# Optimization experiments

Measured on AMD Instinct MI355X. Metric: run time of the kernel, lower is better.

The kernel has to match this reference:

```python
import jax, jax.numpy as jnp
import numpy as np

N, Lq, Lk, D = 4, 2048, 2048, 1024
H, DH = 16, 64  # n_heads, projection_dim
NEG_INF = jnp.float32(-1e30)


def setup_inputs() -> dict:
    key = jax.random.key(0)
    ks = jax.random.split(key, 6)
    query = jax.random.normal(ks[0], (N, Lq, D), dtype=jnp.float32)
    key_t = jax.random.normal(ks[1], (N, Lk, D), dtype=jnp.float32)
    s = 1.0 / np.sqrt(D)
    Wq = jax.random.normal(ks[2], (D, D), dtype=jnp.float32) * s
    Wk = jax.random.normal(ks[3], (D, D), dtype=jnp.float32) * s
    Wv = jax.random.normal(ks[4], (D, D), dtype=jnp.float32) * s
    # causal mask: True where attention is forbidden (j > i)
    mask = jnp.triu(jnp.ones((Lq, Lk), dtype=bool), k=1)
    # per-sample valid lengths in [1024, 2048); padding at the tail
    valid_len = jax.random.randint(ks[5], (N,), Lk // 2, Lk)
    padding_mask = jnp.arange(Lk)[None, :] >= valid_len[:, None]  # (N, Lk) bool
    return {"query": query, "key": key_t, "Wq": Wq, "Wk": Wk, "Wv": Wv,
            "mask": mask, "padding_mask": padding_mask}


def reference(query, key, Wq, Wk, Wv, mask, padding_mask):
    n, lq, _ = query.shape
    lk = key.shape[1]
    # torch Linear (no bias): x @ W.T ; split heads -> (N, H, L, DH)
    q = (query @ Wq.T).reshape(n, lq, H, DH).transpose(0, 2, 1, 3)
    k = (key @ Wk.T).reshape(n, lk, H, DH).transpose(0, 2, 1, 3)
    v = (key @ Wv.T).reshape(n, lk, H, DH).transpose(0, 2, 1, 3)
    # per-sample scaling: sqrt(number of non-padded keys) (module quirk, not sqrt(d))
    valid = jnp.sum(~padding_mask, axis=-1).astype(query.dtype)  # (N,)
    scaling = jnp.sqrt(valid)[:, None, None, None]
    score = jnp.einsum('nhqd,nhkd->nhqk', q, k) / scaling
    score = jnp.where(mask[None, None, :, :], NEG_INF, score)
    score = jnp.where(padding_mask[:, None, None, :], NEG_INF, score)
    attn = jax.nn.softmax(score, axis=-1)
    out = jnp.einsum('nhqk,nhkd->nhqd', attn, v)
    return out.transpose(0, 2, 1, 3).reshape(n, lq, H * DH)
```

## Files before the change

### kernel.cpp

```cpp
#include <hip/hip_runtime.h>
#include <hip/hip_bf16.h>
#include <math.h>


#define N_S 4
#define LQ 2048
#define LK 2048
#define DM 1024
#define NHEAD 16
#define DHEAD 64

typedef __attribute__((ext_vector_type(8))) short short8;
typedef __attribute__((ext_vector_type(4))) float f32x4;

typedef const __attribute__((address_space(1))) void* gptr_t;
typedef __attribute__((address_space(3))) void* lptr_t;

#define GLOAD_LDS(g, l) \
    __builtin_amdgcn_global_load_lds((gptr_t)(const void*)(g), (lptr_t)(void*)(l), 16, 0, 0)

static __device__ __forceinline__ unsigned int pkbf(float a, float b) {
    __hip_bfloat162 h = __float22bfloat162_rn(make_float2(a, b));
    unsigned int u;
    __builtin_memcpy(&u, &h, 4);
    return u;
}

static __device__ __forceinline__ f32x4 zero4() {
    f32x4 v; v[0] = 0.f; v[1] = 0.f; v[2] = 0.f; v[3] = 0.f; return v;
}

__global__ void meta_kernel(const void* __restrict__ pm,
                            int* __restrict__ valid_out,
                            float* __restrict__ scale_out) {
    __shared__ int okInt, hasPair, okF32;
    __shared__ int counts[4];
    int t = threadIdx.x;
    if (t == 0) { okInt = 1; hasPair = 0; okF32 = 1; }
    if (t < 4) counts[t] = 0;
    __syncthreads();

    const unsigned int* w = (const unsigned int*)pm;
    int bad_int = 0, pair = 0, bad_f32 = 0;
    for (int i = t; i < 2048; i += 256) {
        unsigned int v = w[i];
        if (v > 1u) bad_int = 1;
        if (v == 0x3F803F80u) pair = 1;
        if (v != 0u && v != 0x3F800000u) bad_f32 = 1;
    }
    if (bad_int) okInt = 0;
    if (pair)    hasPair = 1;
    if (bad_f32) okF32 = 0;
    __syncthreads();

    int mode = okInt ? 0 : (hasPair ? 1 : (okF32 ? 2 : 3));
    for (int n = 0; n < 4; n++) {
        int cnt = 0;
        for (int j = t; j < LK; j += 256) {
            int idx = n * LK + j;
            bool z;
            if (mode == 0)      z = (((const int*)pm)[idx] == 0);
            else if (mode == 1) z = (((const unsigned short*)pm)[idx] == 0);
            else if (mode == 2) z = (w[idx] == 0u);
            else                z = (((const unsigned char*)pm)[idx] == 0);
            cnt += z ? 1 : 0;
        }
        atomicAdd(&counts[n], cnt);
    }
    __syncthreads();
    if (t < 4) {
        int c = counts[t] > 0 ? counts[t] : 1;
        valid_out[t] = c;
        scale_out[t] = 1.0f / sqrtf((float)c);
    }
}

static __device__ __forceinline__ void conv16(const float* src,
                                              unsigned short* dst, size_t idx) {
    f32x4 a0 = *(const f32x4*)(src + idx);
    f32x4 a1 = *(const f32x4*)(src + idx + 4);
    f32x4 a2 = *(const f32x4*)(src + idx + 8);
    f32x4 a3 = *(const f32x4*)(src + idx + 12);
    uint4 u0, u1;
    u0.x = pkbf(a0[0], a0[1]); u0.y = pkbf(a0[2], a0[3]);
    u0.z = pkbf(a1[0], a1[1]); u0.w = pkbf(a1[2], a1[3]);
    u1.x = pkbf(a2[0], a2[1]); u1.y = pkbf(a2[2], a2[3]);
    u1.z = pkbf(a3[0], a3[1]); u1.w = pkbf(a3[2], a3[3]);
    *(uint4*)(void*)(dst + idx) = u0;
    *(uint4*)(void*)(dst + idx + 8) = u1;
}

__global__ __launch_bounds__(256) void convw_kernel(
    const float* __restrict__ Wq, const float* __restrict__ Wk,
    const float* __restrict__ Wv,
    unsigned short* __restrict__ Wqb, unsigned short* __restrict__ Wkb,
    unsigned short* __restrict__ Wvb)
{
    int z = blockIdx.y;
    const float* src = (z == 0) ? Wq : ((z == 1) ? Wk : Wv);
    unsigned short* dst = (z == 0) ? Wqb : ((z == 1) ? Wkb : Wvb);
    conv16(src, dst, ((size_t)blockIdx.x * 256 + threadIdx.x) * 16);
}

__global__ __launch_bounds__(256) void convx_kernel(
    const float* __restrict__ src, unsigned short* __restrict__ dst)
{
    conv16(src, dst, ((size_t)blockIdx.x * 256 + threadIdx.x) * 16);
}

__global__ __launch_bounds__(256) void convx2_kernel(
    const float* __restrict__ q, const float* __restrict__ k,
    unsigned short* __restrict__ dq, unsigned short* __restrict__ dk)
{
    const float* src = blockIdx.y ? k : q;
    unsigned short* dst = blockIdx.y ? dk : dq;
    conv16(src, dst, ((size_t)blockIdx.x * 256 + threadIdx.x) * 16);
}

__global__ __launch_bounds__(256) void proj_bf16_kernel(
    const unsigned short* __restrict__ XbQ, const unsigned short* __restrict__ XbK,
    const unsigned short* __restrict__ Wqb, const unsigned short* __restrict__ Wkb,
    const unsigned short* __restrict__ Wvb,
    const float* __restrict__ scal,
    unsigned short* __restrict__ Qb, unsigned short* __restrict__ Kb,
    unsigned short* __restrict__ Vt, int zbase)
{
    int z = blockIdx.z + zbase;
    const unsigned short* W = (z == 0) ? Wqb : ((z == 1) ? Wkb : Wvb);
    const unsigned short* Xb = (z == 0) ? XbQ : XbK;

    __shared__ unsigned short Xls[128 * 32];
    __shared__ unsigned short Wls[128 * 32];

    int t = threadIdx.x;
    int wave = t >> 6, lane = t & 63;
    int l15 = lane & 15, quad = lane >> 4;
    int wa = wave >> 1, wb = wave & 1;
    int m0 = blockIdx.x << 7, n0 = blockIdx.y << 7;

    int srow = t >> 2;
    int sg = ((t & 3) ^ (srow & 3)) << 3;
    const unsigned short* gX0 = Xb + (size_t)(m0 + srow) * DM + sg;
    const unsigned short* gX1 = Xb + (size_t)(m0 + 64 + srow) * DM + sg;
    const unsigned short* gW0 = W + (size_t)(n0 + srow) * DM + sg;
    const unsigned short* gW1 = W + (size_t)(n0 + 64 + srow) * DM + sg;

    f32x4 acc[4][4];
    #pragma unroll
    for (int i = 0; i < 4; i++)
        #pragma unroll
        for (int j = 0; j < 4; j++) acc[i][j] = zero4();

    int aoff = ((quad ^ (l15 & 3)) << 3);
    const unsigned short* Abuf = (z < 2) ? Wls : Xls;
    const unsigned short* Bbuf = (z < 2) ? Xls : Wls;

    for (int kk = 0; kk < DM; kk += 32) {
        __syncthreads();
        GLOAD_LDS(gX0 + kk, Xls + wave * 512);
        GLOAD_LDS(gX1 + kk, Xls + 2048 + wave * 512);
        GLOAD_LDS(gW0 + kk, Wls + wave * 512);
        GLOAD_LDS(gW1 + kk, Wls + 2048 + wave * 512);
        __syncthreads();

        short8 af[4], bf[4];
        #pragma unroll
        for (int ai = 0; ai < 4; ai++)
            af[ai] = *(const short8*)(const void*)(
                Abuf + ((wa * 64 + ai * 16 + l15) << 5) + aoff);
        #pragma unroll
        for (int bi = 0; bi < 4; bi++)
            bf[bi] = *(const short8*)(const void*)(
                Bbuf + ((wb * 64 + bi * 16 + l15) << 5) + aoff);
        #pragma unroll
        for (int ai = 0; ai < 4; ai++)
            #pragma unroll
            for (int bi = 0; bi < 4; bi++)
                acc[ai][bi] = __builtin_amdgcn_mfma_f32_16x16x32_bf16(
                    af[ai], bf[bi], acc[ai][bi], 0, 0, 0);
    }

    if (z < 2) {
        unsigned short* O = (z == 0) ? Qb : Kb;
        #pragma unroll
        for (int bi = 0; bi < 4; bi++) {
            int token = m0 + wb * 64 + bi * 16 + l15;
            float qs = 1.0f;
            if (z == 0) qs = scal[token >> 11] * 1.44269504f;
            #pragma unroll
            for (int ai = 0; ai < 4; ai++) {
                int feat = n0 + wa * 64 + ai * 16 + quad * 4;
                float v0 = acc[ai][bi][0], v1 = acc[ai][bi][1];
                float v2 = acc[ai][bi][2], v3 = acc[ai][bi][3];
                if (z == 0) { v0 *= qs; v1 *= qs; v2 *= qs; v3 *= qs; }
                uint2 u;
                u.x = pkbf(v0, v1);
                u.y = pkbf(v2, v3);
                *(uint2*)(void*)(O + (size_t)token * DM + feat) = u;
            }
        }
    } else {
        #pragma unroll
        for (int ai = 0; ai < 4; ai++) {
            int token0 = m0 + wa * 64 + ai * 16 + quad * 4;
            int n = token0 >> 11, tl = token0 & 2047;
            #pragma unroll
            for (int bi = 0; bi < 4; bi++) {
                int feat = n0 + wb * 64 + bi * 16 + l15;
                uint2 u;
                u.x = pkbf(acc[ai][bi][0], acc[ai][bi][1]);
                u.y = pkbf(acc[ai][bi][2], acc[ai][bi][3]);
                *(uint2*)(void*)(Vt + ((size_t)n * DM + feat) * LK + tl) = u;
            }
        }
    }
}

__global__ __launch_bounds__(256) void proj_f32_kernel(
    const float* __restrict__ Xq, const float* __restrict__ Xk,
    const unsigned short* __restrict__ Wqb, const unsigned short* __restrict__ Wkb,
    const unsigned short* __restrict__ Wvb,
    const float* __restrict__ scal,
    unsigned short* __restrict__ Qb, unsigned short* __restrict__ Kb,
    unsigned short* __restrict__ Vt)
{
    int z = blockIdx.z;
    const float* X = (z == 0) ? Xq : Xk;
    const unsigned short* W = (z == 0) ? Wqb : ((z == 1) ? Wkb : Wvb);

    __shared__ unsigned short Xls[128 * 32];
    __shared__ unsigned short Wls[128 * 32];

    int t = threadIdx.x;
    int wave = t >> 6, lane = t & 63;
    int l15 = lane & 15, quad = lane >> 4;
    int wa = wave >> 1, wb = wave & 1;
    int m0 = blockIdx.x << 7, n0 = blockIdx.y << 7;

    int arow = t >> 1, ah = t & 1;
    int ag0 = ((2 * ah)     ^ (arow & 3)) << 3;
    int ag1 = ((2 * ah + 1) ^ (arow & 3)) << 3;
    const float* gX = X + (size_t)(m0 + arow) * DM;
    unsigned short* lX = Xls + arow * 32 + ah * 16;

    int brow = t >> 2;
    int bg = ((t & 3) ^ (brow & 3)) << 3;
    const unsigned short* gW0 = W + (size_t)(n0 + brow) * DM + bg;
    const unsigned short* gW1 = W + (size_t)(n0 + 64 + brow) * DM + bg;

    f32x4 acc[4][4];
    #pragma unroll
    for (int i = 0; i < 4; i++)
        #pragma unroll
        for (int j = 0; j < 4; j++) acc[i][j] = zero4();

    int aoff = ((quad ^ (l15 & 3)) << 3);

    f32x4 an0 = *(const f32x4*)(gX + ag0);
    f32x4 an1 = *(const f32x4*)(gX + ag0 + 4);
    f32x4 an2 = *(const f32x4*)(gX + ag1);
    f32x4 an3 = *(const f32x4*)(gX + ag1 + 4);

    const unsigned short* Abuf = (z < 2) ? Wls : Xls;
    const unsigned short* Bbuf = (z < 2) ? Xls : Wls;

    for (int kk = 0; kk < DM; kk += 32) {
        __syncthreads();
        GLOAD_LDS(gW0 + kk, Wls + wave * 512);
        GLOAD_LDS(gW1 + kk, Wls + 2048 + wave * 512);
        uint4 ua, ub;
        ua.x = pkbf(an0[0], an0[1]); ua.y = pkbf(an0[2], an0[3]);
        ua.z = pkbf(an1[0], an1[1]); ua.w = pkbf(an1[2], an1[3]);
        ub.x = pkbf(an2[0], an2[1]); ub.y = pkbf(an2[2], an2[3]);
        ub.z = pkbf(an3[0], an3[1]); ub.w = pkbf(an3[2], an3[3]);
        *(uint4*)(void*)(lX)     = ua;
        *(uint4*)(void*)(lX + 8) = ub;
        __syncthreads();

        if (kk + 32 < DM) {
            an0 = *(const f32x4*)(gX + kk + 32 + ag0);
            an1 = *(const f32x4*)(gX + kk + 32 + ag0 + 4);
            an2 = *(const f32x4*)(gX + kk + 32 + ag1);
            an3 = *(const f32x4*)(gX + kk + 32 + ag1 + 4);
        }

        short8 af[4], bf[4];
        #pragma unroll
        for (int ai = 0; ai < 4; ai++)
            af[ai] = *(const short8*)(const void*)(
                Abuf + ((wa * 64 + ai * 16 + l15) << 5) + aoff);
        #pragma unroll
        for (int bi = 0; bi < 4; bi++)
            bf[bi] = *(const short8*)(const void*)(
                Bbuf + ((wb * 64 + bi * 16 + l15) << 5) + aoff);
        #pragma unroll
        for (int ai = 0; ai < 4; ai++)
            #pragma unroll
            for (int bi = 0; bi < 4; bi++)
                acc[ai][bi] = __builtin_amdgcn_mfma_f32_16x16x32_bf16(
                    af[ai], bf[bi], acc[ai][bi], 0, 0, 0);
    }

    if (z < 2) {
        unsigned short* O = (z == 0) ? Qb : Kb;
        #pragma unroll
        for (int bi = 0; bi < 4; bi++) {
            int token = m0 + wb * 64 + bi * 16 + l15;
            float qs = 1.0f;
            if (z == 0) qs = scal[token >> 11] * 1.44269504f;
            #pragma unroll
            for (int ai = 0; ai < 4; ai++) {
                int feat = n0 + wa * 64 + ai * 16 + quad * 4;
                float v0 = acc[ai][bi][0], v1 = acc[ai][bi][1];
                float v2 = acc[ai][bi][2], v3 = acc[ai][bi][3];
                if (z == 0) { v0 *= qs; v1 *= qs; v2 *= qs; v3 *= qs; }
                uint2 u;
                u.x = pkbf(v0, v1);
                u.y = pkbf(v2, v3);
                *(uint2*)(void*)(O + (size_t)token * DM + feat) = u;
            }
        }
    } else {
        #pragma unroll
        for (int ai = 0; ai < 4; ai++) {
            int token0 = m0 + wa * 64 + ai * 16 + quad * 4;
            int n = token0 >> 11, tl = token0 & 2047;
            #pragma unroll
            for (int bi = 0; bi < 4; bi++) {
                int feat = n0 + wb * 64 + bi * 16 + l15;
                uint2 u;
                u.x = pkbf(acc[ai][bi][0], acc[ai][bi][1]);
                u.y = pkbf(acc[ai][bi][2], acc[ai][bi][3]);
                *(uint2*)(void*)(Vt + ((size_t)n * DM + feat) * LK + tl) = u;
            }
        }
    }
}

__global__ __launch_bounds__(256) void attn_kernel(
    const unsigned short* __restrict__ Qb, const unsigned short* __restrict__ Kb,
    const unsigned short* __restrict__ Vt,
    const int* __restrict__ valid_arr,
    float* __restrict__ out)
{
    __shared__ unsigned short Kls[2][64 * 64];

    int bx = blockIdx.x;
    int nh = blockIdx.y;
    int n = nh >> 4, h = nh & 15;
    int tA = bx, tB = 31 - bx;

    int valid = valid_arr[n];
    int tvalid = (valid + 63) >> 6;
    int TlA = (tA + 1 < tvalid) ? tA + 1 : tvalid;
    int TlB = (tB + 1 < tvalid) ? tB + 1 : tvalid;

    int t = threadIdx.x;
    int wave = t >> 6, lane = t & 63;
    int l15 = lane & 15, quad = lane >> 4;

    int qyA = tA * 64 + wave * 16 + l15;
    int qyB = tB * 64 + wave * 16 + l15;
    int qw0A = tA * 64 + wave * 16;
    int qw0B = tB * 64 + wave * 16;

    const unsigned short* QrowA = Qb + ((size_t)n * LQ + qyA) * DM + h * DHEAD;
    const unsigned short* QrowB = Qb + ((size_t)n * LQ + qyB) * DM + h * DHEAD;
    short8 qfA0 = *(const short8*)(const void*)(QrowA + quad * 8);
    short8 qfA1 = *(const short8*)(const void*)(QrowA + 32 + quad * 8);
    short8 qfB0 = *(const short8*)(const void*)(QrowB + quad * 8);
    short8 qfB1 = *(const short8*)(const void*)(QrowB + 32 + quad * 8);

    f32x4 OA[4], OB[4];
    #pragma unroll
    for (int i = 0; i < 4; i++) { OA[i] = zero4(); OB[i] = zero4(); }
    f32x4 LAcc = zero4(), LBcc = zero4();

    short8 onesf;
    #pragma unroll
    for (int i = 0; i < 8; i++) onesf[i] = (short)0x3F80;

    const unsigned short* Kbase = Kb + (size_t)n * LK * DM + h * DHEAD;
    const unsigned short* Vbase = Vt + ((size_t)n * DM + h * DHEAD) * LK;

    int srow0 = t >> 3;
    int sgk   = (((t & 7) ^ (srow0 & 7)) << 3);

    GLOAD_LDS(Kbase + (size_t)srow0 * DM + sgk,        &Kls[0][0] + wave * 512);
    GLOAD_LDS(Kbase + (size_t)(32 + srow0) * DM + sgk, &Kls[0][0] + 2048 + wave * 512);

    for (int kt = 0; kt < TlB; kt++) {
        int jb = kt << 6;
        int cur = kt & 1;
        bool doA = (kt < TlA);

        __syncthreads();

        f32x4 sA[4], sB[4];
        #pragma unroll
        for (int cb = 0; cb < 4; cb++) {
            const unsigned short* krow = &Kls[cur][0] + ((cb * 16 + l15) << 6);
            short8 kf0 = *(const short8*)(const void*)(krow + ((quad ^ (l15 & 7)) << 3));
            short8 kf1 = *(const short8*)(const void*)(krow + (((4 + quad) ^ (l15 & 7)) << 3));
            f32x4 sb = zero4();
            sb = __builtin_amdgcn_mfma_f32_16x16x32_bf16(kf0, qfB0, sb, 0, 0, 0);
            sb = __builtin_amdgcn_mfma_f32_16x16x32_bf16(kf1, qfB1, sb, 0, 0, 0);
            sB[cb] = sb;
            if (doA) {
                f32x4 sa = zero4();
                sa = __builtin_amdgcn_mfma_f32_16x16x32_bf16(kf0, qfA0, sa, 0, 0, 0);
                sa = __builtin_amdgcn_mfma_f32_16x16x32_bf16(kf1, qfA1, sa, 0, 0, 0);
                sA[cb] = sa;
            }
        }

        short8 vf0[4], vf1[4];
        #pragma unroll
        for (int cb = 0; cb < 4; cb++) {
            vf0[cb] = *(const short8*)(const void*)(
                Vbase + (size_t)(cb * 16 + l15) * LK + jb + quad * 8);
            vf1[cb] = *(const short8*)(const void*)(
                Vbase + (size_t)(cb * 16 + l15) * LK + jb + 32 + quad * 8);
        }
        if (kt + 1 < TlB) {
            int jb2 = jb + 64;
            GLOAD_LDS(Kbase + (size_t)(jb2 + srow0) * DM + sgk,
                      &Kls[1 - cur][0] + wave * 512);
            GLOAD_LDS(Kbase + (size_t)(jb2 + 32 + srow0) * DM + sgk,
                      &Kls[1 - cur][0] + 2048 + wave * 512);
        }

        if (jb + 63 > qw0B || jb + 64 > valid) {
            #pragma unroll
            for (int cb = 0; cb < 4; cb++) {
                int jb2 = jb + cb * 16 + quad * 4;
                #pragma unroll
                for (int r = 0; r < 4; r++) {
                    int j = jb2 + r;
                    if (j > qyB || j >= valid) sB[cb][r] = -1e30f;
                }
            }
        }
        short8 pfB0, pfB1;
        {
            unsigned int lo[4], hi[4];
            #pragma unroll
            for (int cb = 0; cb < 4; cb++) {
                lo[cb] = pkbf(__builtin_amdgcn_exp2f(sB[cb][0]),
                              __builtin_amdgcn_exp2f(sB[cb][1]));
                hi[cb] = pkbf(__builtin_amdgcn_exp2f(sB[cb][2]),
                              __builtin_amdgcn_exp2f(sB[cb][3]));
            }
            asm("v_permlane32_swap_b32 %0, %1" : "+v"(lo[0]), "+v"(lo[1]));
            asm("v_permlane32_swap_b32 %0, %1" : "+v"(hi[0]), "+v"(hi[1]));
            asm("v_permlane32_swap_b32 %0, %1" : "+v"(lo[2]), "+v"(lo[3]));
            asm("v_permlane32_swap_b32 %0, %1" : "+v"(hi[2]), "+v"(hi[3]));
            asm("v_permlane16_swap_b32 %0, %1" : "+v"(lo[0]), "+v"(lo[1]));
            asm("v_permlane16_swap_b32 %0, %1" : "+v"(hi[0]), "+v"(hi[1]));
            asm("v_permlane16_swap_b32 %0, %1" : "+v"(lo[2]), "+v"(lo[3]));
            asm("v_permlane16_swap_b32 %0, %1" : "+v"(hi[2]), "+v"(hi[3]));
            uint4 w0, w1;
            w0.x = lo[0]; w0.y = hi[0]; w0.z = lo[1]; w0.w = hi[1];
            w1.x = lo[2]; w1.y = hi[2]; w1.z = lo[3]; w1.w = hi[3];
            __builtin_memcpy(&pfB0, &w0, 16);
            __builtin_memcpy(&pfB1, &w1, 16);
        }

        #pragma unroll
        for (int cb = 0; cb < 4; cb++) {
            OB[cb] = __builtin_amdgcn_mfma_f32_16x16x32_bf16(pfB0, vf0[cb], OB[cb], 0, 0, 0);
            OB[cb] = __builtin_amdgcn_mfma_f32_16x16x32_bf16(pfB1, vf1[cb], OB[cb], 0, 0, 0);
        }
        LBcc = __builtin_amdgcn_mfma_f32_16x16x32_bf16(pfB0, onesf, LBcc, 0, 0, 0);
        LBcc = __builtin_amdgcn_mfma_f32_16x16x32_bf16(pfB1, onesf, LBcc, 0, 0, 0);

        if (doA) {
            if (jb + 63 > qw0A || jb + 64 > valid) {
                #pragma unroll
                for (int cb = 0; cb < 4; cb++) {
                    int jb2 = jb + cb * 16 + quad * 4;
                    #pragma unroll
                    for (int r = 0; r < 4; r++) {
                        int j = jb2 + r;
                        if (j > qyA || j >= valid) sA[cb][r] = -1e30f;
                    }
                }
            }
            short8 pfA0, pfA1;
            {
                unsigned int lo[4], hi[4];
                #pragma unroll
                for (int cb = 0; cb < 4; cb++) {
                    lo[cb] = pkbf(__builtin_amdgcn_exp2f(sA[cb][0]),
                                  __builtin_amdgcn_exp2f(sA[cb][1]));
                    hi[cb] = pkbf(__builtin_amdgcn_exp2f(sA[cb][2]),
                                  __builtin_amdgcn_exp2f(sA[cb][3]));
                }
                asm("v_permlane32_swap_b32 %0, %1" : "+v"(lo[0]), "+v"(lo[1]));
                asm("v_permlane32_swap_b32 %0, %1" : "+v"(hi[0]), "+v"(hi[1]));
                asm("v_permlane32_swap_b32 %0, %1" : "+v"(lo[2]), "+v"(lo[3]));
                asm("v_permlane32_swap_b32 %0, %1" : "+v"(hi[2]), "+v"(hi[3]));
                asm("v_permlane16_swap_b32 %0, %1" : "+v"(lo[0]), "+v"(lo[1]));
                asm("v_permlane16_swap_b32 %0, %1" : "+v"(hi[0]), "+v"(hi[1]));
                asm("v_permlane16_swap_b32 %0, %1" : "+v"(lo[2]), "+v"(lo[3]));
                asm("v_permlane16_swap_b32 %0, %1" : "+v"(hi[2]), "+v"(hi[3]));
                uint4 w0, w1;
                w0.x = lo[0]; w0.y = hi[0]; w0.z = lo[1]; w0.w = hi[1];
                w1.x = lo[2]; w1.y = hi[2]; w1.z = lo[3]; w1.w = hi[3];
                __builtin_memcpy(&pfA0, &w0, 16);
                __builtin_memcpy(&pfA1, &w1, 16);
            }
            #pragma unroll
            for (int cb = 0; cb < 4; cb++) {
                OA[cb] = __builtin_amdgcn_mfma_f32_16x16x32_bf16(pfA0, vf0[cb], OA[cb], 0, 0, 0);
                OA[cb] = __builtin_amdgcn_mfma_f32_16x16x32_bf16(pfA1, vf1[cb], OA[cb], 0, 0, 0);
            }
            LAcc = __builtin_amdgcn_mfma_f32_16x16x32_bf16(pfA0, onesf, LAcc, 0, 0, 0);
            LAcc = __builtin_amdgcn_mfma_f32_16x16x32_bf16(pfA1, onesf, LAcc, 0, 0, 0);
        }
    }

    float* obase = out + ((size_t)n * LQ) * DM + h * DHEAD;
    #pragma unroll
    for (int r = 0; r < 4; r++) {
        float iA = 1.0f / LAcc[r];
        float iB = 1.0f / LBcc[r];
        int rowA = tA * 64 + wave * 16 + quad * 4 + r;
        int rowB = tB * 64 + wave * 16 + quad * 4 + r;
        #pragma unroll
        for (int cb = 0; cb < 4; cb++) {
            obase[(size_t)rowA * DM + cb * 16 + l15] = OA[cb][r] * iA;
            obase[(size_t)rowB * DM + cb * 16 + l15] = OB[cb][r] * iB;
        }
    }
}

extern "C" void kernel_launch(void* const* d_in, const int* in_sizes, int n_in,
                              void* d_out, int out_size, void* d_ws, size_t ws_size,
                              hipStream_t stream)
{
    (void)in_sizes; (void)n_in; (void)out_size;

    const float* query = (const float*)d_in[0];
    const float* key   = (const float*)d_in[1];
    const float* Wq    = (const float*)d_in[2];
    const float* Wk    = (const float*)d_in[3];
    const float* Wv    = (const float*)d_in[4];
    const void* pmask  = d_in[6];

    char* ws = (char*)d_ws;
    unsigned short* Qb  = (unsigned short*)(ws);
    unsigned short* Kb  = (unsigned short*)(ws + (size_t)16 * 1024 * 1024);
    unsigned short* Vt  = (unsigned short*)(ws + (size_t)32 * 1024 * 1024);
    int*   valid = (int*)  (ws + (size_t)48 * 1024 * 1024);
    float* scal  = (float*)(ws + (size_t)48 * 1024 * 1024 + 64);
    unsigned short* Wqb = (unsigned short*)(ws + (size_t)48 * 1024 * 1024 + 4096);
    unsigned short* Wkb = Wqb + (size_t)DM * DM;
    unsigned short* Wvb = Wkb + (size_t)DM * DM;
    unsigned short* XbQ = Wvb + (size_t)DM * DM;
    unsigned short* XbK = XbQ + (size_t)N_S * LQ * DM;

    size_t xbytes      = (size_t)N_S * LQ * DM * 2;
    size_t need_phased = (size_t)(48 * 1024 * 1024) + 4096
                       + 3 * (size_t)DM * DM * 2 + xbytes;
    size_t need_full   = need_phased + xbytes;

    meta_kernel<<<1, 256, 0, stream>>>(pmask, valid, scal);
    convw_kernel<<<dim3(256, 3), 256, 0, stream>>>(Wq, Wk, Wv, Wqb, Wkb, Wvb);

    if (ws_size >= need_full) {
        convx2_kernel<<<dim3(2048, 2), 256, 0, stream>>>(query, key, XbQ, XbK);
        proj_bf16_kernel<<<dim3(64, 8, 3), 256, 0, stream>>>(
            XbQ, XbK, Wqb, Wkb, Wvb, scal, Qb, Kb, Vt, 0);
    } else if (ws_size >= need_phased) {
        convx_kernel<<<2048, 256, 0, stream>>>(query, XbQ);
        proj_bf16_kernel<<<dim3(64, 8, 1), 256, 0, stream>>>(
            XbQ, XbQ, Wqb, Wkb, Wvb, scal, Qb, Kb, Vt, 0);
        convx_kernel<<<2048, 256, 0, stream>>>(key, XbQ);
        proj_bf16_kernel<<<dim3(64, 8, 2), 256, 0, stream>>>(
            XbQ, XbQ, Wqb, Wkb, Wvb, scal, Qb, Kb, Vt, 1);
    } else {
        proj_f32_kernel<<<dim3(64, 8, 3), 256, 0, stream>>>(
            query, key, Wqb, Wkb, Wvb, scal, Qb, Kb, Vt);
    }

    attn_kernel<<<dim3(16, 64), 256, 0, stream>>>(Qb, Kb, Vt, valid,
                                                  (float*)d_out);
}
```

Baseline: 334.6 us.

## Triple-buffer K tiles in attention and fuse prep kernels into one launch

Attention now uses three LDS buffers for K tiles, so the load for the tile two iterations ahead is issued while the current one is computed. The full __syncthreads is replaced with a raw s_barrier, and s_setprio is raised around the MFMA blocks. The meta, weight-convert and input-convert kernels are merged into one prep launch to cut launch overhead. The raw barrier has no explicit vmcnt wait inside the loop, which risks reading K tiles before their loads complete.

```diff
diff --git a/kernel.cpp b/kernel.cpp
--- a/kernel.cpp
+++ b/kernel.cpp
@@ -30,9 +30,9 @@
     f32x4 v; v[0] = 0.f; v[1] = 0.f; v[2] = 0.f; v[3] = 0.f; return v;
 }
 
-__global__ void meta_kernel(const void* __restrict__ pm,
-                            int* __restrict__ valid_out,
-                            float* __restrict__ scale_out) {
+static __device__ __forceinline__ void meta_body(const void* __restrict__ pm,
+                                                 int* __restrict__ valid_out,
+                                                 float* __restrict__ scale_out) {
     __shared__ int okInt, hasPair, okF32;
     __shared__ int counts[4];
     int t = threadIdx.x;
@@ -73,6 +73,12 @@
         valid_out[t] = c;
         scale_out[t] = 1.0f / sqrtf((float)c);
     }
+}
+
+__global__ void meta_kernel(const void* __restrict__ pm,
+                            int* __restrict__ valid_out,
+                            float* __restrict__ scale_out) {
+    meta_body(pm, valid_out, scale_out);
 }
 
 static __device__ __forceinline__ void conv16(const float* src,
@@ -108,13 +114,33 @@
     conv16(src, dst, ((size_t)blockIdx.x * 256 + threadIdx.x) * 16);
 }
 
-__global__ __launch_bounds__(256) void convx2_kernel(
-    const float* __restrict__ q, const float* __restrict__ k,
+__global__ __launch_bounds__(256) void prep_kernel(
+    const void* __restrict__ pm, int* __restrict__ valid_out,
+    float* __restrict__ scale_out,
+    const float* __restrict__ Wq, const float* __restrict__ Wk,
+    const float* __restrict__ Wv,
+    unsigned short* __restrict__ Wqb, unsigned short* __restrict__ Wkb,
+    unsigned short* __restrict__ Wvb,
+    const float* __restrict__ xq, const float* __restrict__ xk,
     unsigned short* __restrict__ dq, unsigned short* __restrict__ dk)
 {
-    const float* src = blockIdx.y ? k : q;
-    unsigned short* dst = blockIdx.y ? dk : dq;
-    conv16(src, dst, ((size_t)blockIdx.x * 256 + threadIdx.x) * 16);
+    int b = blockIdx.x;
+    int t = threadIdx.x;
+    if (b == 0) {
+        meta_body(pm, valid_out, scale_out);
+    } else if (b <= 768) {
+        int bb = b - 1;
+        int z = bb >> 8;
+        const float* src = (z == 0) ? Wq : ((z == 1) ? Wk : Wv);
+        unsigned short* dst = (z == 0) ? Wqb : ((z == 1) ? Wkb : Wvb);
+        conv16(src, dst, ((size_t)(bb & 255) * 256 + t) * 16);
+    } else {
+        int bb = b - 769;
+        const float* src = (bb >= 2048) ? xk : xq;
+        unsigned short* dst = (bb >= 2048) ? dk : dq;
+        int x = (bb >= 2048) ? bb - 2048 : bb;
+        conv16(src, dst, ((size_t)x * 256 + t) * 16);
+    }
 }
 
 __global__ __launch_bounds__(256) void proj_bf16_kernel(
@@ -343,7 +369,7 @@
     const int* __restrict__ valid_arr,
     float* __restrict__ out)
 {
-    __shared__ unsigned short Kls[2][64 * 64];
+    __shared__ unsigned short Kls[3][64 * 64];
 
     int bx = blockIdx.x;
     int nh = blockIdx.y;
@@ -388,15 +414,28 @@
 
     GLOAD_LDS(Kbase + (size_t)srow0 * DM + sgk,        &Kls[0][0] + wave * 512);
     GLOAD_LDS(Kbase + (size_t)(32 + srow0) * DM + sgk, &Kls[0][0] + 2048 + wave * 512);
-
+    if (TlB > 1) {
+        GLOAD_LDS(Kbase + (size_t)(64 + srow0) * DM + sgk,
+                  &Kls[1][0] + wave * 512);
+        GLOAD_LDS(Kbase + (size_t)(96 + srow0) * DM + sgk,
+                  &Kls[1][0] + 2048 + wave * 512);
+        asm volatile("s_waitcnt vmcnt(2)" ::: "memory");
+    } else {
+        asm volatile("s_waitcnt vmcnt(0)" ::: "memory");
+    }
+
+    int cur = 0;
     for (int kt = 0; kt < TlB; kt++) {
         int jb = kt << 6;
-        int cur = kt & 1;
         bool doA = (kt < TlA);
-
-        __syncthreads();
+        int nxt = (cur == 0) ? 2 : cur - 1;
+
+        __builtin_amdgcn_sched_barrier(0);
+        __builtin_amdgcn_s_barrier();
+        __builtin_amdgcn_sched_barrier(0);
 
         f32x4 sA[4], sB[4];
+        __builtin_amdgcn_s_setprio(1);
         #pragma unroll
         for (int cb = 0; cb < 4; cb++) {
             const unsigned short* krow = &Kls[cur][0] + ((cb * 16 + l15) << 6);
@@ -413,6 +452,7 @@
                 sA[cb] = sa;
             }
         }
+        __builtin_amdgcn_s_setprio(0);
 
         short8 vf0[4], vf1[4];
         #pragma unroll
@@ -422,12 +462,12 @@
             vf1[cb] = *(const short8*)(const void*)(
                 Vbase + (size_t)(cb * 16 + l15) * LK + jb + 32 + quad * 8);
         }
-        if (kt + 1 < TlB) {
-            int jb2 = jb + 64;
+        if (kt + 2 < TlB) {
+            int jb2 = jb + 128;
             GLOAD_LDS(Kbase + (size_t)(jb2 + srow0) * DM + sgk,
-                      &Kls[1 - cur][0] + wave * 512);
+                      &Kls[nxt][0] + wave * 512);
             GLOAD_LDS(Kbase + (size_t)(jb2 + 32 + srow0) * DM + sgk,
-                      &Kls[1 - cur][0] + 2048 + wave * 512);
+                      &Kls[nxt][0] + 2048 + wave * 512);
         }
 
         if (jb + 63 > qw0B || jb + 64 > valid) {
@@ -466,6 +506,7 @@
             __builtin_memcpy(&pfB1, &w1, 16);
         }
 
+        __builtin_amdgcn_s_setprio(1);
         #pragma unroll
         for (int cb = 0; cb < 4; cb++) {
             OB[cb] = __builtin_amdgcn_mfma_f32_16x16x32_bf16(pfB0, vf0[cb], OB[cb], 0, 0, 0);
@@ -473,6 +514,7 @@
         }
         LBcc = __builtin_amdgcn_mfma_f32_16x16x32_bf16(pfB0, onesf, LBcc, 0, 0, 0);
         LBcc = __builtin_amdgcn_mfma_f32_16x16x32_bf16(pfB1, onesf, LBcc, 0, 0, 0);
+        __builtin_amdgcn_s_setprio(0);
 
         if (doA) {
             if (jb + 63 > qw0A || jb + 64 > valid) {
@@ -510,6 +552,7 @@
                 __builtin_memcpy(&pfA0, &w0, 16);
                 __builtin_memcpy(&pfA1, &w1, 16);
             }
+            __builtin_amdgcn_s_setprio(1);
             #pragma unroll
             for (int cb = 0; cb < 4; cb++) {
                 OA[cb] = __builtin_amdgcn_mfma_f32_16x16x32_bf16(pfA0, vf0[cb], OA[cb], 0, 0, 0);
@@ -517,7 +560,10 @@
             }
             LAcc = __builtin_amdgcn_mfma_f32_16x16x32_bf16(pfA0, onesf, LAcc, 0, 0, 0);
             LAcc = __builtin_amdgcn_mfma_f32_16x16x32_bf16(pfA1, onesf, LAcc, 0, 0, 0);
-        }
+            __builtin_amdgcn_s_setprio(0);
+        }
+
+        cur = (cur == 2) ? 0 : cur + 1;
     }
 
     float* obase = out + ((size_t)n * LQ) * DM + h * DHEAD;
@@ -565,14 +611,15 @@
                        + 3 * (size_t)DM * DM * 2 + xbytes;
     size_t need_full   = need_phased + xbytes;
 
-    meta_kernel<<<1, 256, 0, stream>>>(pmask, valid, scal);
-    convw_kernel<<<dim3(256, 3), 256, 0, stream>>>(Wq, Wk, Wv, Wqb, Wkb, Wvb);
-
     if (ws_size >= need_full) {
-        convx2_kernel<<<dim3(2048, 2), 256, 0, stream>>>(query, key, XbQ, XbK);
+        prep_kernel<<<dim3(1 + 768 + 4096), 256, 0, stream>>>(
+            pmask, valid, scal, Wq, Wk, Wv, Wqb, Wkb, Wvb,
+            query, key, XbQ, XbK);
         proj_bf16_kernel<<<dim3(64, 8, 3), 256, 0, stream>>>(
             XbQ, XbK, Wqb, Wkb, Wvb, scal, Qb, Kb, Vt, 0);
     } else if (ws_size >= need_phased) {
+        meta_kernel<<<1, 256, 0, stream>>>(pmask, valid, scal);
+        convw_kernel<<<dim3(256, 3), 256, 0, stream>>>(Wq, Wk, Wv, Wqb, Wkb, Wvb);
         convx_kernel<<<2048, 256, 0, stream>>>(query, XbQ);
         proj_bf16_kernel<<<dim3(64, 8, 1), 256, 0, stream>>>(
             XbQ, XbQ, Wqb, Wkb, Wvb, scal, Qb, Kb, Vt, 0);
@@ -580,6 +627,8 @@
         proj_bf16_kernel<<<dim3(64, 8, 2), 256, 0, stream>>>(
             XbQ, XbQ, Wqb, Wkb, Wvb, scal, Qb, Kb, Vt, 1);
     } else {
+        meta_kernel<<<1, 256, 0, stream>>>(pmask, valid, scal);
+        convw_kernel<<<dim3(256, 3), 256, 0, stream>>>(Wq, Wk, Wv, Wqb, Wkb, Wvb);
         proj_f32_kernel<<<dim3(64, 8, 3), 256, 0, stream>>>(
             query, key, Wqb, Wkb, Wvb, scal, Qb, Kb, Vt);
     }
```

Result: no change. 331.6 us (-0.9%).
